# Kernel optimization log

Hardware: AMD Instinct MI355X
Metric: run time of the kernel (lower is better)

The kernel has to match this reference:

```python
import jax, jax.numpy as jnp
import numpy as np

HIDDEN = 2048
FFN = 1024
NUM_EXPERTS = 64
TOP_K = 8
TOTAL_EXPERTS = NUM_EXPERTS + TOP_K  # trash-can experts appended


def setup_inputs() -> dict:
    key = jax.random.key(0)
    ks = jax.random.split(key, 5)
    hidden_states = jax.random.normal(ks[0], (4, 2048, HIDDEN), dtype=jnp.float32)
    # gate: [total_experts, hidden]
    gate_w = jax.random.normal(ks[1], (TOTAL_EXPERTS, HIDDEN), dtype=jnp.float32) * 0.02
    # OlmoeMLP (SwiGLU): gate_proj, up_proj: [E, hidden, ffn]; down_proj: [E, ffn, hidden]
    w_gate = jax.random.normal(ks[2], (NUM_EXPERTS, HIDDEN, FFN), dtype=jnp.float32) * 0.02
    w_up = jax.random.normal(ks[3], (NUM_EXPERTS, HIDDEN, FFN), dtype=jnp.float32) * 0.02
    w_down = jax.random.normal(ks[4], (NUM_EXPERTS, FFN, HIDDEN), dtype=jnp.float32) * 0.02
    return {"hidden_states": hidden_states, "gate_w": gate_w,
            "w_gate": w_gate, "w_up": w_up, "w_down": w_down}


def _moe_forward(hidden_states, gate_w, w_gate, w_up, w_down):
    b, s, h = hidden_states.shape
    x = hidden_states.reshape(-1, h)  # [T, H]
    router_logits = x @ gate_w.T  # [T, total_experts]
    routing_weights = jax.nn.softmax(router_logits.astype(jnp.float32), axis=-1)
    topk_w, topk_idx = jax.lax.top_k(routing_weights, TOP_K)  # [T, K]
    # norm_topk_prob = False -> no renorm
    topk_w = topk_w.astype(hidden_states.dtype)

    # Dense-equivalent combine honoring sparsity via per-expert mask-weighted sum:
    # combine_w[t, e] = sum of topk weights where topk_idx==e, zero for trash experts.
    onehot = jax.nn.one_hot(topk_idx, TOTAL_EXPERTS, dtype=topk_w.dtype)  # [T,K,E_tot]
    combine_w = jnp.einsum('tk,tke->te', topk_w, onehot)[:, :NUM_EXPERTS]  # [T,E]

    # Grouped expert compute (vectorized over experts).
    # For correctness baseline we compute each expert on all tokens and weight;
    # zero weights kill non-routed tokens (same math as gather/scatter).
    def one_expert(wg, wu, wd, w_col):
        inter = jax.nn.silu(x @ wg) * (x @ wu)  # [T, FFN]
        return (inter @ wd) * w_col[:, None]    # [T, H]

    out = jnp.zeros_like(x)
    # scan over experts to cap peak memory at one [T,FFN] intermediate
    def body(acc, args):
        wg, wu, wd, w_col = args
        return acc + one_expert(wg, wu, wd, w_col), None
    out, _ = jax.lax.scan(body, out, (w_gate, w_up, w_down, combine_w.T))
    return out.reshape(b, s, h), router_logits


def reference(hidden_states, gate_w, w_gate, w_up, w_down):
    return _moe_forward(hidden_states, gate_w, w_gate, w_up, w_down)
```

## Files before the change

### kernel.cpp

```cpp
#include <hip/hip_runtime.h>
#include <hip/hip_bf16.h>
#include <stdint.h>

#define T_TOK 8192
#define HID   2048
#define FFN   1024
#define NEXP  64
#define ETOT  72
#define NPAD  80
#define TOPK  8
#define NASSIGN (T_TOK*TOPK)

typedef unsigned short u16;
typedef __bf16 bf16;
typedef bf16 bf16x8 __attribute__((ext_vector_type(8)));
typedef float f32x4 __attribute__((ext_vector_type(4)));

typedef const __attribute__((address_space(1))) void* gp_t;
typedef __attribute__((address_space(3))) void* lp_t;

__device__ __forceinline__ void gload16(const void* g, void* lds) {
  __builtin_amdgcn_global_load_lds((gp_t)g, (lp_t)lds, 16, 0, 0);
}
__device__ __forceinline__ f32x4 mfma16(bf16x8 a, bf16x8 b, f32x4 c) {
  return __builtin_amdgcn_mfma_f32_16x16x32_bf16(a, b, c, 0, 0, 0);
}

union U8 { bf16 h[8]; uint4 u; };
union U2 { bf16 h[2]; unsigned int u; };

__global__ void k_prep_x(const float* __restrict__ x, u16* __restrict__ xh,
                         u16* __restrict__ xl, int n8) {
  int i = blockIdx.x * blockDim.x + threadIdx.x;
  int stride = gridDim.x * blockDim.x;
  for (; i < n8; i += stride) {
    const float4* p = (const float4*)(x + (size_t)i * 8);
    float4 a = p[0], b = p[1];
    float f[8] = {a.x,a.y,a.z,a.w,b.x,b.y,b.z,b.w};
    U8 hh, ll;
#pragma unroll
    for (int j = 0; j < 8; j++) {
      bf16 h = (bf16)f[j];
      hh.h[j] = h;
      ll.h[j] = (bf16)(f[j] - (float)h);
    }
    ((uint4*)xh)[i] = hh.u;
    ((uint4*)xl)[i] = ll.u;
  }
}

__global__ void k_prep_gate(const float* __restrict__ gw, u16* __restrict__ gh,
                            u16* __restrict__ gl) {
  int e = blockIdx.x;
  for (int k8 = threadIdx.x; k8 < HID/8; k8 += blockDim.x) {
    U8 hh, ll;
    if (e < ETOT) {
      const float4* p = (const float4*)(gw + (size_t)e*HID + k8*8);
      float4 a = p[0], b = p[1];
      float f[8] = {a.x,a.y,a.z,a.w,b.x,b.y,b.z,b.w};
#pragma unroll
      for (int j = 0; j < 8; j++) {
        bf16 h = (bf16)f[j]; hh.h[j] = h; ll.h[j] = (bf16)(f[j]-(float)h);
      }
    } else {
      hh.u = make_uint4(0,0,0,0); ll.u = make_uint4(0,0,0,0);
    }
    ((uint4*)gh)[(size_t)e*(HID/8) + k8] = hh.u;
    ((uint4*)gl)[(size_t)e*(HID/8) + k8] = ll.u;
  }
}

__global__ void k_convT(const float* __restrict__ src, u16* __restrict__ dst,
                        int R, int C) {
  int e = blockIdx.z;
  src += (size_t)e * R * C;
  dst += (size_t)e * R * C;
  int c0 = blockIdx.x * 64, r0 = blockIdx.y * 128;
  __shared__ u16 t[64 * 132];
  int tid = threadIdx.x;
  int rr = tid >> 4, cc = (tid & 15) * 4;
#pragma unroll
  for (int it = 0; it < 8; it++) {
    int r = it * 16 + rr;
    float4 v = *(const float4*)(src + (size_t)(r0 + r) * C + c0 + cc);
    const float* f = &v.x;
#pragma unroll
    for (int i = 0; i < 4; i++) {
      U2 u; u.h[0] = (bf16)f[i]; u.h[1] = (bf16)0.f;
      t[(cc + i) * 132 + r] = (u16)(u.u & 0xffffu);
    }
  }
  __syncthreads();
  int n = tid >> 2, kb = (tid & 3) * 32;
  u16* drow = dst + (size_t)(c0 + n) * R + r0 + kb;
  const u16* srow = &t[n * 132 + kb];
#pragma unroll
  for (int j = 0; j < 2; j++) {
    uint2 a = *(const uint2*)&srow[j*16 + 0];
    uint2 b = *(const uint2*)&srow[j*16 + 4];
    uint2 c = *(const uint2*)&srow[j*16 + 8];
    uint2 d = *(const uint2*)&srow[j*16 + 12];
    *(uint4*)&drow[j*16]     = make_uint4(a.x, a.y, b.x, b.y);
    *(uint4*)&drow[j*16 + 8] = make_uint4(c.x, c.y, d.x, d.y);
  }
}

__global__ void k_router(const u16* __restrict__ xh, const u16* __restrict__ xl,
                         const u16* __restrict__ gh, const u16* __restrict__ gl,
                         float* __restrict__ logits_out, int* __restrict__ tk_idx,
                         float* __restrict__ tk_w, int* __restrict__ counts) {
  __shared__ u16 la_h[64*32], la_l[64*32], lb_h[NPAD*32], lb_l[NPAD*32];
  __shared__ float llog[64*NPAD];
  int tid = threadIdx.x, lane = tid & 63, wid = tid >> 6;
  int t0 = blockIdx.x * 64;
  int rsub = lane >> 2, csub = lane & 3;
  f32x4 acc[5] = {};
#pragma unroll 1
  for (int k0 = 0; k0 < HID; k0 += 32) {
    int arow = wid*16 + rsub;
    gload16(xh + (size_t)(t0+arow)*HID + k0 + csub*8, &la_h[wid*512]);
    gload16(xl + (size_t)(t0+arow)*HID + k0 + csub*8, &la_l[wid*512]);
    int brow = wid*16 + rsub;
    gload16(gh + (size_t)brow*HID + k0 + csub*8, &lb_h[wid*512]);
    gload16(gl + (size_t)brow*HID + k0 + csub*8, &lb_l[wid*512]);
    if (wid == 0) gload16(gh + (size_t)(64+rsub)*HID + k0 + csub*8, &lb_h[4*512]);
    if (wid == 1) gload16(gl + (size_t)(64+rsub)*HID + k0 + csub*8, &lb_l[4*512]);
    __syncthreads();
    int ar = wid*16 + (lane & 15);
    int ks = lane >> 4;
    bf16x8 ah = *(const bf16x8*)&la_h[ar*32 + ks*8];
    bf16x8 al = *(const bf16x8*)&la_l[ar*32 + ks*8];
#pragma unroll
    for (int nf = 0; nf < 5; nf++) {
      int br = nf*16 + (lane & 15);
      bf16x8 bh = *(const bf16x8*)&lb_h[br*32 + ks*8];
      bf16x8 bl = *(const bf16x8*)&lb_l[br*32 + ks*8];
      acc[nf] = mfma16(ah, bh, acc[nf]);
      acc[nf] = mfma16(ah, bl, acc[nf]);
      acc[nf] = mfma16(al, bh, acc[nf]);
    }
    __syncthreads();
  }
  {
    int q = lane >> 4, c = lane & 15;
#pragma unroll
    for (int nf = 0; nf < 5; nf++)
#pragma unroll
      for (int r = 0; r < 4; r++)
        llog[(wid*16 + q*4 + r)*NPAD + nf*16 + c] = acc[nf][r];
  }
  __syncthreads();
  if (tid < 64) {
    int t = t0 + tid;
    float* lg = &llog[tid*NPAD];
    float m = -1e30f;
    for (int e = 0; e < ETOT; e++) {
      float v = lg[e];
      logits_out[(size_t)t*ETOT + e] = v;
      m = fmaxf(m, v);
    }
    float s = 0.f;
    for (int e = 0; e < ETOT; e++) s += __expf(lg[e] - m);
    uint64_t m0 = 0; unsigned int m1 = 0;
    for (int k = 0; k < TOPK; k++) {
      float best = -1e30f; int bi = 0;
      for (int e = 0; e < ETOT; e++) {
        bool used = (e < 64) ? ((m0 >> e) & 1) : ((m1 >> (e-64)) & 1);
        float v = lg[e];
        if (!used && v > best) { best = v; bi = e; }
      }
      if (bi < 64) m0 |= (1ull << bi); else m1 |= (1u << (bi-64));
      tk_idx[t*TOPK + k] = bi;
      tk_w[t*TOPK + k] = __expf(best - m) / s;
      if (bi < NEXP) atomicAdd(&counts[bi], 1);
    }
  }
}

__global__ void k_scan(const int* __restrict__ counts, int* __restrict__ offsets,
                       int* __restrict__ cursors) {
  if (threadIdx.x == 0) {
    int s = 0;
    for (int e = 0; e < NEXP; e++) { offsets[e] = s; cursors[e] = s; s += counts[e]; }
  }
}

__global__ void k_build(const int* __restrict__ tk_idx, const float* __restrict__ tk_w,
                        int* __restrict__ cursors, int* __restrict__ rows,
                        float* __restrict__ rwgt, int* __restrict__ slots) {
  int t = blockIdx.x * blockDim.x + threadIdx.x;
  if (t >= T_TOK) return;
#pragma unroll
  for (int k = 0; k < TOPK; k++) {
    int e = tk_idx[t*TOPK + k];
    if (e < NEXP) {
      int p = atomicAdd(&cursors[e], 1);
      rows[p] = t;
      rwgt[p] = tk_w[t*TOPK + k];
      slots[t*TOPK + k] = p;
    } else {
      slots[t*TOPK + k] = -1;
    }
  }
}

#define FRAG_COMPUTE(LAP, LBP) do { \
    bf16x8 afr[4], bfr[4]; \
    _Pragma("unroll") \
    for (int i = 0; i < 4; i++) { \
      int row = wm + i*16 + (lane & 15); \
      int ch = (lane >> 4) ^ ((row >> 1) & 3); \
      afr[i] = *(const bf16x8*)&(LAP)[row*32 + ch*8]; \
      int n = wn + i*16 + (lane & 15); \
      int chb = (lane >> 4) ^ ((n >> 1) & 3); \
      bfr[i] = *(const bf16x8*)&(LBP)[n*32 + chb*8]; \
    } \
    _Pragma("unroll") \
    for (int nf = 0; nf < 4; nf++) \
      _Pragma("unroll") \
      for (int mf = 0; mf < 4; mf++) \
        acc[mf][nf] = mfma16(afr[mf], bfr[nf], acc[mf][nf]); \
  } while (0)

#define BK64_LOOP(KDIM) \
    _Pragma("unroll 1") \
    for (int k0 = 0; k0 < (KDIM); k0 += 64) { \
      gload16(ga1 + k0, &la[wid*512]); \
      gload16(ga2 + k0, &la[(wid+4)*512]); \
      gload16(gb1 + k0, &lb[wid*512]); \
      gload16(gb2 + k0, &lb[(wid+4)*512]); \
      gload16(ga1 + k0 + 32, &la[4096 + wid*512]); \
      gload16(ga2 + k0 + 32, &la[4096 + (wid+4)*512]); \
      gload16(gb1 + k0 + 32, &lb[4096 + wid*512]); \
      gload16(gb2 + k0 + 32, &lb[4096 + (wid+4)*512]); \
      __syncthreads(); \
      FRAG_COMPUTE(la, lb); \
      FRAG_COMPUTE((la + 4096), (lb + 4096)); \
      __syncthreads(); \
    }

__launch_bounds__(256, 4)
__global__ void k_gate(const u16* __restrict__ xh, const u16* __restrict__ wT,
                       const int* __restrict__ counts, const int* __restrict__ offsets,
                       const int* __restrict__ rows, u16* __restrict__ gout) {
  int wgid = blockIdx.x;
  int xcd = wgid & 7, slot = wgid >> 3;
  int m = slot & 7, q = slot >> 3;
  int g = xcd * 64 + q;
  int e = g >> 3, nb = g & 7;
  int cnt = counts[e];
  if (cnt == 0) return;
  int off = offsets[e];
  int n0 = nb * 128;
  int tid = threadIdx.x, lane = tid & 63, wid = tid >> 6;
  int wm = (wid >> 1) * 64, wn = (wid & 1) * 64;
  __shared__ __align__(16) char smem[32768];
  u16* la = (u16*)smem;
  u16* lb = (u16*)(smem + 16384);
  u16* lout = (u16*)smem;
  int rsub = lane >> 2, csub = lane & 3;
  int swzc = csub ^ ((rsub >> 1) & 3);
  int nr1 = wid*16 + rsub, nr2 = nr1 + 64;
  const u16* gb1 = wT + ((size_t)e*FFN + n0 + nr1)*HID + swzc*8;
  const u16* gb2 = wT + ((size_t)e*FFN + n0 + nr2)*HID + swzc*8;

  for (int m0 = m * 128; m0 < cnt; m0 += 1024) {
    int tok1 = (m0 + nr1 < cnt) ? rows[off + m0 + nr1] : 0;
    int tok2 = (m0 + nr2 < cnt) ? rows[off + m0 + nr2] : 0;
    const u16* ga1 = xh + (size_t)tok1*HID + swzc*8;
    const u16* ga2 = xh + (size_t)tok2*HID + swzc*8;
    f32x4 acc[4][4] = {};
    BK64_LOOP(HID)
#pragma unroll
    for (int pass = 0; pass < 2; pass++) {
      if ((wid >> 1) == pass) {
#pragma unroll
        for (int mf = 0; mf < 4; mf++)
#pragma unroll
          for (int nf = 0; nf < 4; nf++)
#pragma unroll
            for (int r = 0; r < 4; r++) {
              int row = mf*16 + (lane >> 4)*4 + r;
              int col = wn + nf*16 + (lane & 15);
              U2 t; t.h[0] = (bf16)acc[mf][nf][r]; t.h[1] = (bf16)0.f;
              lout[row*128 + col] = (u16)(t.u & 0xffffu);
            }
      }
      __syncthreads();
      for (int idx = tid; idx < 1024; idx += 256) {
        int row = idx >> 4, c16 = idx & 15;
        int grow = m0 + pass*64 + row;
        if (grow < cnt) {
          uint4 v = *(const uint4*)&lout[row*128 + c16*8];
          *(uint4*)&gout[(size_t)(off + grow)*FFN + n0 + c16*8] = v;
        }
      }
      __syncthreads();
    }
  }
}

__launch_bounds__(256, 4)
__global__ void k_up(const u16* __restrict__ xh, const u16* __restrict__ wT,
                     const int* __restrict__ counts, const int* __restrict__ offsets,
                     const int* __restrict__ rows, u16* __restrict__ inter) {
  int wgid = blockIdx.x;
  int xcd = wgid & 7, slot = wgid >> 3;
  int m = slot & 7, q = slot >> 3;
  int g = xcd * 64 + q;
  int e = g >> 3, nb = g & 7;
  int cnt = counts[e];
  if (cnt == 0) return;
  int off = offsets[e];
  int n0 = nb * 128;
  int tid = threadIdx.x, lane = tid & 63, wid = tid >> 6;
  int wm = (wid >> 1) * 64, wn = (wid & 1) * 64;
  __shared__ __align__(16) char smem[32768];
  u16* la = (u16*)smem;
  u16* lb = (u16*)(smem + 16384);
  u16* lg = (u16*)smem;
  u16* lout = (u16*)(smem + 16384);
  int rsub = lane >> 2, csub = lane & 3;
  int swzc = csub ^ ((rsub >> 1) & 3);
  int nr1 = wid*16 + rsub, nr2 = nr1 + 64;
  const u16* gb1 = wT + ((size_t)e*FFN + n0 + nr1)*HID + swzc*8;
  const u16* gb2 = wT + ((size_t)e*FFN + n0 + nr2)*HID + swzc*8;

  for (int m0 = m * 128; m0 < cnt; m0 += 1024) {
    int tok1 = (m0 + nr1 < cnt) ? rows[off + m0 + nr1] : 0;
    int tok2 = (m0 + nr2 < cnt) ? rows[off + m0 + nr2] : 0;
    const u16* ga1 = xh + (size_t)tok1*HID + swzc*8;
    const u16* ga2 = xh + (size_t)tok2*HID + swzc*8;
    f32x4 acc[4][4] = {};
    BK64_LOOP(HID)
#pragma unroll
    for (int pass = 0; pass < 2; pass++) {
      for (int idx = tid; idx < 1024; idx += 256) {
        int row = idx >> 4, c16 = idx & 15;
        int grow = m0 + pass*64 + row;
        uint4 v = make_uint4(0,0,0,0);
        if (grow < cnt)
          v = *(const uint4*)&inter[(size_t)(off + grow)*FFN + n0 + c16*8];
        *(uint4*)&lg[row*128 + c16*8] = v;
      }
      __syncthreads();
      if ((wid >> 1) == pass) {
#pragma unroll
        for (int mf = 0; mf < 4; mf++)
#pragma unroll
          for (int nf = 0; nf < 4; nf++)
#pragma unroll
            for (int r = 0; r < 4; r++) {
              int row = mf*16 + (lane >> 4)*4 + r;
              int col = wn + nf*16 + (lane & 15);
              U2 gv; gv.u = (unsigned int)lg[row*128 + col];
              float gg = (float)gv.h[0];
              float v = gg / (1.f + __expf(-gg)) * acc[mf][nf][r];
              U2 t; t.h[0] = (bf16)v; t.h[1] = (bf16)0.f;
              lout[row*128 + col] = (u16)(t.u & 0xffffu);
            }
      }
      __syncthreads();
      for (int idx = tid; idx < 1024; idx += 256) {
        int row = idx >> 4, c16 = idx & 15;
        int grow = m0 + pass*64 + row;
        if (grow < cnt) {
          uint4 v = *(const uint4*)&lout[row*128 + c16*8];
          *(uint4*)&inter[(size_t)(off + grow)*FFN + n0 + c16*8] = v;
        }
      }
      __syncthreads();
    }
  }
}

__launch_bounds__(256, 4)
__global__ void k_expert_down(const u16* __restrict__ inter, const u16* __restrict__ wdT,
                              const int* __restrict__ counts, const int* __restrict__ offsets,
                              const float* __restrict__ rwgt, u16* __restrict__ dscratch) {
  int wgid = blockIdx.x;
  int xcd = wgid & 7, slot = wgid >> 3;
  int m = slot & 3, q = slot >> 2;
  int g = xcd * 128 + q;
  int e = g >> 4, nb = g & 15;
  int cnt = counts[e];
  if (cnt == 0) return;
  int off = offsets[e];
  int n0 = nb * 128;
  int tid = threadIdx.x, lane = tid & 63, wid = tid >> 6;
  int wm = (wid >> 1) * 64, wn = (wid & 1) * 64;
  __shared__ __align__(16) char smem[32768];
  u16* la = (u16*)smem;
  u16* lb = (u16*)(smem + 16384);
  u16* lout = (u16*)smem;
  __shared__ float rw_l[128];
  int rsub = lane >> 2, csub = lane & 3;
  int swzc = csub ^ ((rsub >> 1) & 3);
  int nr1 = wid*16 + rsub, nr2 = nr1 + 64;
  const u16* gb1 = wdT + ((size_t)e*HID + n0 + nr1)*FFN + swzc*8;
  const u16* gb2 = wdT + ((size_t)e*HID + n0 + nr2)*FFN + swzc*8;

  for (int m0 = m * 128; m0 < cnt; m0 += 512) {
    __syncthreads();
    if (tid < 128) {
      int r = m0 + tid;
      rw_l[tid] = (r < cnt) ? rwgt[off + r] : 0.f;
    }
    const u16* ga1 = inter + (size_t)(off + m0 + nr1)*FFN + swzc*8;
    const u16* ga2 = inter + (size_t)(off + m0 + nr2)*FFN + swzc*8;
    f32x4 acc[4][4] = {};
    BK64_LOOP(FFN)
#pragma unroll
    for (int pass = 0; pass < 2; pass++) {
      if ((wid >> 1) == pass) {
#pragma unroll
        for (int mf = 0; mf < 4; mf++)
#pragma unroll
          for (int nf = 0; nf < 4; nf++)
#pragma unroll
            for (int r = 0; r < 4; r++) {
              int row = mf*16 + (lane >> 4)*4 + r;
              int col = wn + nf*16 + (lane & 15);
              float w = rw_l[pass*64 + row];
              U2 t; t.h[0] = (bf16)(w * acc[mf][nf][r]); t.h[1] = (bf16)0.f;
              lout[row*128 + col] = (u16)(t.u & 0xffffu);
            }
      }
      __syncthreads();
      for (int idx = tid; idx < 1024; idx += 256) {
        int row = idx >> 4, c16 = idx & 15;
        int grow = m0 + pass*64 + row;
        if (grow < cnt) {
          uint4 v = *(const uint4*)&lout[row*128 + c16*8];
          *(uint4*)&dscratch[(size_t)(off + grow)*HID + n0 + c16*8] = v;
        }
      }
      __syncthreads();
    }
  }
}

__global__ void k_combine(const u16* __restrict__ dscratch, const int* __restrict__ slots,
                          float* __restrict__ out) {
  int t = blockIdx.x;
  int tid = threadIdx.x;
  __shared__ int sl[TOPK];
  if (tid < TOPK) sl[tid] = slots[t*TOPK + tid];
  __syncthreads();
  int c = tid * 8;
  float acc[8] = {0.f,0.f,0.f,0.f,0.f,0.f,0.f,0.f};
#pragma unroll
  for (int k = 0; k < TOPK; k++) {
    int p = sl[k];
    if (p >= 0) {
      bf16x8 v = *(const bf16x8*)&dscratch[(size_t)p*HID + c];
#pragma unroll
      for (int i = 0; i < 8; i++) acc[i] += (float)v[i];
    }
  }
  float4 o0 = make_float4(acc[0], acc[1], acc[2], acc[3]);
  float4 o1 = make_float4(acc[4], acc[5], acc[6], acc[7]);
  *(float4*)&out[(size_t)t*HID + c]     = o0;
  *(float4*)&out[(size_t)t*HID + c + 4] = o1;
}

extern "C" void kernel_launch(void* const* d_in, const int* in_sizes, int n_in,
                              void* d_out, int out_size, void* d_ws, size_t ws_size,
                              hipStream_t stream) {
  const float* x      = (const float*)d_in[0];
  const float* gate_w = (const float*)d_in[1];
  const float* wg     = (const float*)d_in[2];
  const float* wu     = (const float*)d_in[3];
  const float* wd     = (const float*)d_in[4];
  float* out = (float*)d_out;
  float* logits_out = out + (size_t)T_TOK * HID;

  char* w = (char*)d_ws;
  u16* xh = (u16*)w;            w += (size_t)T_TOK*HID*2;
  u16* xl = (u16*)w;            w += (size_t)T_TOK*HID*2;
  u16* gh = (u16*)w;            w += (size_t)NPAD*HID*2;
  u16* gl = (u16*)w;            w += (size_t)NPAD*HID*2;
  int* tk_idx = (int*)w;        w += (size_t)T_TOK*TOPK*4;
  float* tk_w = (float*)w;      w += (size_t)T_TOK*TOPK*4;
  int* counts = (int*)w;        w += 256;
  int* offsets = (int*)w;       w += 256;
  int* cursors = (int*)w;       w += 256;
  int* rows = (int*)w;          w += (size_t)NASSIGN*4;
  float* rwgt = (float*)w;      w += (size_t)NASSIGN*4;
  int* slots = (int*)w;         w += (size_t)NASSIGN*4;
  u16* inter = (u16*)w;         w += ((size_t)NASSIGN + 256)*FFN*2;
  u16* dscratch = (u16*)w;      w += (size_t)NASSIGN*HID*2;
  u16* wgT = (u16*)w;           w += (size_t)NEXP*FFN*HID*2;
  u16* wuT = (u16*)w;           w += (size_t)NEXP*FFN*HID*2;
  u16* wdT = (u16*)w;

  hipMemsetAsync(counts, 0, 256, stream);

  k_prep_x<<<2048, 256, 0, stream>>>(x, xh, xl, T_TOK*HID/8);
  k_prep_gate<<<NPAD, 256, 0, stream>>>(gate_w, gh, gl);
  k_router<<<T_TOK/64, 256, 0, stream>>>(xh, xl, gh, gl, logits_out, tk_idx, tk_w, counts);
  k_scan<<<1, 64, 0, stream>>>(counts, offsets, cursors);
  k_build<<<T_TOK/256, 256, 0, stream>>>(tk_idx, tk_w, cursors, rows, rwgt, slots);

  k_convT<<<dim3(FFN/64, HID/128, NEXP), 256, 0, stream>>>(wg, wgT, HID, FFN);
  k_convT<<<dim3(FFN/64, HID/128, NEXP), 256, 0, stream>>>(wu, wuT, HID, FFN);
  k_convT<<<dim3(HID/64, FFN/128, NEXP), 256, 0, stream>>>(wd, wdT, FFN, HID);

  k_gate<<<4096, 256, 0, stream>>>(xh, wgT, counts, offsets, rows, inter);
  k_up<<<4096, 256, 0, stream>>>(xh, wuT, counts, offsets, rows, inter);
  k_expert_down<<<4096, 256, 0, stream>>>(inter, wdT, counts, offsets, rwgt, dscratch);
  k_combine<<<T_TOK, 256, 0, stream>>>(dscratch, slots, out);
}
```

Measured before the change: 1.762 ms.

## Fuse weight transpose-conversion into router and expert GEMM kernels for overlap

Removes the three standalone weight conversion kernels. Their tiles are folded into the preceding compute kernels as extra workgroups: router plus gate-weight conversion, gate GEMM plus up-weight conversion, up GEMM plus down-weight conversion. This lets memory-bound conversion overlap with compute-bound work and drops launch gaps. It also switches the conversion to nontemporal loads and stores. The cost is interleaved block scheduling, which can contend for bandwidth and occupancy with the GEMM blocks, and the router's launch bounds drop to 2.

```diff
diff --git a/kernel.cpp b/kernel.cpp
--- a/kernel.cpp
+++ b/kernel.cpp
@@ -15,6 +15,7 @@
 typedef __bf16 bf16;
 typedef bf16 bf16x8 __attribute__((ext_vector_type(8)));
 typedef float f32x4 __attribute__((ext_vector_type(4)));
+typedef unsigned int u32x4 __attribute__((ext_vector_type(4)));
 
 typedef const __attribute__((address_space(1))) void* gp_t;
 typedef __attribute__((address_space(3))) void* lp_t;
@@ -28,6 +29,52 @@
 
 union U8 { bf16 h[8]; uint4 u; };
 union U2 { bf16 h[2]; unsigned int u; };
+union UV { u32x4 v; float f[4]; };
+
+__device__ __forceinline__ void conv_tile4(const float* __restrict__ src0,
+                                           u16* __restrict__ dst0,
+                                           int R, int C, int conv_id, u16* t) {
+  int tid = threadIdx.x;
+  int tiles_c = C >> 6;
+  int rr = tid >> 4, cc = (tid & 15) * 4;
+#pragma unroll 1
+  for (int j = 0; j < 4; j++) {
+    int tile = conv_id * 4 + j;
+    int e = tile >> 8, rem = tile & 255;
+    int bx = rem % tiles_c, by = rem / tiles_c;
+    const float* src = src0 + (size_t)e * R * C;
+    u16* dst = dst0 + (size_t)e * R * C;
+    int c0 = bx * 64, r0 = by * 128;
+    __syncthreads();
+#pragma unroll
+    for (int it = 0; it < 8; it++) {
+      int r = it * 16 + rr;
+      UV uv;
+      uv.v = __builtin_nontemporal_load(
+          (const u32x4*)(src + (size_t)(r0 + r) * C + c0 + cc));
+#pragma unroll
+      for (int i = 0; i < 4; i++) {
+        U2 u; u.h[0] = (bf16)uv.f[i]; u.h[1] = (bf16)0.f;
+        t[(cc + i) * 132 + r] = (u16)(u.u & 0xffffu);
+      }
+    }
+    __syncthreads();
+    int n = tid >> 2, kb = (tid & 3) * 32;
+    u16* drow = dst + (size_t)(c0 + n) * R + r0 + kb;
+    const u16* srow = &t[n * 132 + kb];
+#pragma unroll
+    for (int jj = 0; jj < 2; jj++) {
+      uint2 a = *(const uint2*)&srow[jj*16 + 0];
+      uint2 b = *(const uint2*)&srow[jj*16 + 4];
+      uint2 c = *(const uint2*)&srow[jj*16 + 8];
+      uint2 d = *(const uint2*)&srow[jj*16 + 12];
+      u32x4 o0 = {a.x, a.y, b.x, b.y};
+      u32x4 o1 = {c.x, c.y, d.x, d.y};
+      __builtin_nontemporal_store(o0, (u32x4*)&drow[jj*16]);
+      __builtin_nontemporal_store(o1, (u32x4*)&drow[jj*16 + 8]);
+    }
+  }
+}
 
 __global__ void k_prep_x(const float* __restrict__ x, u16* __restrict__ xh,
                          u16* __restrict__ xl, int n8) {
@@ -70,49 +117,25 @@
   }
 }
 
-__global__ void k_convT(const float* __restrict__ src, u16* __restrict__ dst,
-                        int R, int C) {
-  int e = blockIdx.z;
-  src += (size_t)e * R * C;
-  dst += (size_t)e * R * C;
-  int c0 = blockIdx.x * 64, r0 = blockIdx.y * 128;
-  __shared__ u16 t[64 * 132];
-  int tid = threadIdx.x;
-  int rr = tid >> 4, cc = (tid & 15) * 4;
-#pragma unroll
-  for (int it = 0; it < 8; it++) {
-    int r = it * 16 + rr;
-    float4 v = *(const float4*)(src + (size_t)(r0 + r) * C + c0 + cc);
-    const float* f = &v.x;
-#pragma unroll
-    for (int i = 0; i < 4; i++) {
-      U2 u; u.h[0] = (bf16)f[i]; u.h[1] = (bf16)0.f;
-      t[(cc + i) * 132 + r] = (u16)(u.u & 0xffffu);
-    }
-  }
-  __syncthreads();
-  int n = tid >> 2, kb = (tid & 3) * 32;
-  u16* drow = dst + (size_t)(c0 + n) * R + r0 + kb;
-  const u16* srow = &t[n * 132 + kb];
-#pragma unroll
-  for (int j = 0; j < 2; j++) {
-    uint2 a = *(const uint2*)&srow[j*16 + 0];
-    uint2 b = *(const uint2*)&srow[j*16 + 4];
-    uint2 c = *(const uint2*)&srow[j*16 + 8];
-    uint2 d = *(const uint2*)&srow[j*16 + 12];
-    *(uint4*)&drow[j*16]     = make_uint4(a.x, a.y, b.x, b.y);
-    *(uint4*)&drow[j*16 + 8] = make_uint4(c.x, c.y, d.x, d.y);
-  }
-}
-
-__global__ void k_router(const u16* __restrict__ xh, const u16* __restrict__ xl,
-                         const u16* __restrict__ gh, const u16* __restrict__ gl,
-                         float* __restrict__ logits_out, int* __restrict__ tk_idx,
-                         float* __restrict__ tk_w, int* __restrict__ counts) {
-  __shared__ u16 la_h[64*32], la_l[64*32], lb_h[NPAD*32], lb_l[NPAD*32];
-  __shared__ float llog[64*NPAD];
+__launch_bounds__(256, 2)
+__global__ void k_router_convwg(const u16* __restrict__ xh, const u16* __restrict__ xl,
+                                const u16* __restrict__ gh, const u16* __restrict__ gl,
+                                float* __restrict__ logits_out, int* __restrict__ tk_idx,
+                                float* __restrict__ tk_w, int* __restrict__ counts,
+                                const float* __restrict__ wg_src, u16* __restrict__ wgT) {
+  __shared__ __align__(16) char smem[38912];
+  int bid = blockIdx.x;
+  if (bid >= 128) {
+    conv_tile4(wg_src, wgT, HID, FFN, bid - 128, (u16*)smem);
+    return;
+  }
+  u16* la_h = (u16*)smem;
+  u16* la_l = (u16*)(smem + 4096);
+  u16* lb_h = (u16*)(smem + 8192);
+  u16* lb_l = (u16*)(smem + 13312);
+  float* llog = (float*)(smem + 18432);
   int tid = threadIdx.x, lane = tid & 63, wid = tid >> 6;
-  int t0 = blockIdx.x * 64;
+  int t0 = bid * 64;
   int rsub = lane >> 2, csub = lane & 3;
   f32x4 acc[5] = {};
 #pragma unroll 1
@@ -240,10 +263,18 @@
     }
 
 __launch_bounds__(256, 4)
-__global__ void k_gate(const u16* __restrict__ xh, const u16* __restrict__ wT,
-                       const int* __restrict__ counts, const int* __restrict__ offsets,
-                       const int* __restrict__ rows, u16* __restrict__ gout) {
-  int wgid = blockIdx.x;
+__global__ void k_gate_convwu(const u16* __restrict__ xh, const u16* __restrict__ wT,
+                              const int* __restrict__ counts, const int* __restrict__ offsets,
+                              const int* __restrict__ rows, u16* __restrict__ gout,
+                              const float* __restrict__ wu_src, u16* __restrict__ wuT) {
+  __shared__ __align__(16) char smem[32768];
+  int bid = blockIdx.x;
+  int octet = bid >> 3, lane8 = bid & 7;
+  if (octet & 1) {
+    conv_tile4(wu_src, wuT, HID, FFN, ((octet >> 1) << 3) | lane8, (u16*)smem);
+    return;
+  }
+  int wgid = ((octet >> 1) << 3) | lane8;
   int xcd = wgid & 7, slot = wgid >> 3;
   int m = slot & 7, q = slot >> 3;
   int g = xcd * 64 + q;
@@ -254,7 +285,6 @@
   int n0 = nb * 128;
   int tid = threadIdx.x, lane = tid & 63, wid = tid >> 6;
   int wm = (wid >> 1) * 64, wn = (wid & 1) * 64;
-  __shared__ __align__(16) char smem[32768];
   u16* la = (u16*)smem;
   u16* lb = (u16*)(smem + 16384);
   u16* lout = (u16*)smem;
@@ -301,10 +331,18 @@
 }
 
 __launch_bounds__(256, 4)
-__global__ void k_up(const u16* __restrict__ xh, const u16* __restrict__ wT,
-                     const int* __restrict__ counts, const int* __restrict__ offsets,
-                     const int* __restrict__ rows, u16* __restrict__ inter) {
-  int wgid = blockIdx.x;
+__global__ void k_up_convwd(const u16* __restrict__ xh, const u16* __restrict__ wT,
+                            const int* __restrict__ counts, const int* __restrict__ offsets,
+                            const int* __restrict__ rows, u16* __restrict__ inter,
+                            const float* __restrict__ wd_src, u16* __restrict__ wdT) {
+  __shared__ __align__(16) char smem[32768];
+  int bid = blockIdx.x;
+  int octet = bid >> 3, lane8 = bid & 7;
+  if (octet & 1) {
+    conv_tile4(wd_src, wdT, FFN, HID, ((octet >> 1) << 3) | lane8, (u16*)smem);
+    return;
+  }
+  int wgid = ((octet >> 1) << 3) | lane8;
   int xcd = wgid & 7, slot = wgid >> 3;
   int m = slot & 7, q = slot >> 3;
   int g = xcd * 64 + q;
@@ -315,7 +353,6 @@
   int n0 = nb * 128;
   int tid = threadIdx.x, lane = tid & 63, wid = tid >> 6;
   int wm = (wid >> 1) * 64, wn = (wid & 1) * 64;
-  __shared__ __align__(16) char smem[32768];
   u16* la = (u16*)smem;
   u16* lb = (u16*)(smem + 16384);
   u16* lg = (u16*)smem;
@@ -498,16 +535,13 @@
 
   k_prep_x<<<2048, 256, 0, stream>>>(x, xh, xl, T_TOK*HID/8);
   k_prep_gate<<<NPAD, 256, 0, stream>>>(gate_w, gh, gl);
-  k_router<<<T_TOK/64, 256, 0, stream>>>(xh, xl, gh, gl, logits_out, tk_idx, tk_w, counts);
+  k_router_convwg<<<128 + 4096, 256, 0, stream>>>(
+      xh, xl, gh, gl, logits_out, tk_idx, tk_w, counts, wg, wgT);
   k_scan<<<1, 64, 0, stream>>>(counts, offsets, cursors);
   k_build<<<T_TOK/256, 256, 0, stream>>>(tk_idx, tk_w, cursors, rows, rwgt, slots);
 
-  k_convT<<<dim3(FFN/64, HID/128, NEXP), 256, 0, stream>>>(wg, wgT, HID, FFN);
-  k_convT<<<dim3(FFN/64, HID/128, NEXP), 256, 0, stream>>>(wu, wuT, HID, FFN);
-  k_convT<<<dim3(HID/64, FFN/128, NEXP), 256, 0, stream>>>(wd, wdT, FFN, HID);
-
-  k_gate<<<4096, 256, 0, stream>>>(xh, wgT, counts, offsets, rows, inter);
-  k_up<<<4096, 256, 0, stream>>>(xh, wuT, counts, offsets, rows, inter);
+  k_gate_convwu<<<8192, 256, 0, stream>>>(xh, wgT, counts, offsets, rows, inter, wu, wuT);
+  k_up_convwd<<<8192, 256, 0, stream>>>(xh, wuT, counts, offsets, rows, inter, wd, wdT);
   k_expert_down<<<4096, 256, 0, stream>>>(inter, wdT, counts, offsets, rwgt, dscratch);
   k_combine<<<T_TOK, 256, 0, stream>>>(dscratch, slots, out);
 }
```

Result: slower. 2.499 ms (+41.8%).

## Double-buffer K-loop with async LDS prefetch and vmcnt waits

Applied to the files above, without the earlier changes.

Replaces the synchronous BK=64 loop, which loads both halves and then computes, with a BK=32 double-buffered pipeline in all three grouped GEMM kernels. The next K-slice is issued into the alternate LDS buffer before computing the current one, and explicit s_waitcnt vmcnt(4) waits only for the older loads. This aims to overlap global-to-LDS transfer with MFMA work, at the cost of twice as many barriers per unit of K and reliance on manual vmcnt accounting for correctness.

```diff
diff --git a/kernel.cpp b/kernel.cpp
--- a/kernel.cpp
+++ b/kernel.cpp
@@ -222,22 +222,30 @@
         acc[mf][nf] = mfma16(afr[mf], bfr[nf], acc[mf][nf]); \
   } while (0)
 
-#define BK64_LOOP(KDIM) \
+#define STAGE32(B, K0) do { \
+    gload16(ga1 + (K0), &la[(B)*4096 + wid*512]); \
+    gload16(ga2 + (K0), &la[(B)*4096 + (wid+4)*512]); \
+    gload16(gb1 + (K0), &lb[(B)*4096 + wid*512]); \
+    gload16(gb2 + (K0), &lb[(B)*4096 + (wid+4)*512]); \
+  } while (0)
+
+#define BK32_PIPE(KDIM) do { \
+    int b = 0; \
+    STAGE32(0, 0); \
     _Pragma("unroll 1") \
-    for (int k0 = 0; k0 < (KDIM); k0 += 64) { \
-      gload16(ga1 + k0, &la[wid*512]); \
-      gload16(ga2 + k0, &la[(wid+4)*512]); \
-      gload16(gb1 + k0, &lb[wid*512]); \
-      gload16(gb2 + k0, &lb[(wid+4)*512]); \
-      gload16(ga1 + k0 + 32, &la[4096 + wid*512]); \
-      gload16(ga2 + k0 + 32, &la[4096 + (wid+4)*512]); \
-      gload16(gb1 + k0 + 32, &lb[4096 + wid*512]); \
-      gload16(gb2 + k0 + 32, &lb[4096 + (wid+4)*512]); \
-      __syncthreads(); \
-      FRAG_COMPUTE(la, lb); \
-      FRAG_COMPUTE((la + 4096), (lb + 4096)); \
-      __syncthreads(); \
-    }
+    for (int k0 = 0; k0 < (KDIM); k0 += 32) { \
+      if (k0 + 32 < (KDIM)) { \
+        STAGE32(b ^ 1, k0 + 32); \
+        asm volatile("s_waitcnt vmcnt(4)" ::: "memory"); \
+      } else { \
+        asm volatile("s_waitcnt vmcnt(0)" ::: "memory"); \
+      } \
+      __builtin_amdgcn_s_barrier(); \
+      FRAG_COMPUTE((la + b*4096), (lb + b*4096)); \
+      __builtin_amdgcn_s_barrier(); \
+      b ^= 1; \
+    } \
+  } while (0)
 
 __launch_bounds__(256, 4)
 __global__ void k_gate(const u16* __restrict__ xh, const u16* __restrict__ wT,
@@ -270,7 +278,8 @@
     const u16* ga1 = xh + (size_t)tok1*HID + swzc*8;
     const u16* ga2 = xh + (size_t)tok2*HID + swzc*8;
     f32x4 acc[4][4] = {};
-    BK64_LOOP(HID)
+    BK32_PIPE(HID);
+    __syncthreads();
 #pragma unroll
     for (int pass = 0; pass < 2; pass++) {
       if ((wid >> 1) == pass) {
@@ -332,7 +341,8 @@
     const u16* ga1 = xh + (size_t)tok1*HID + swzc*8;
     const u16* ga2 = xh + (size_t)tok2*HID + swzc*8;
     f32x4 acc[4][4] = {};
-    BK64_LOOP(HID)
+    BK32_PIPE(HID);
+    __syncthreads();
 #pragma unroll
     for (int pass = 0; pass < 2; pass++) {
       for (int idx = tid; idx < 1024; idx += 256) {
@@ -409,7 +419,8 @@
     const u16* ga1 = inter + (size_t)(off + m0 + nr1)*FFN + swzc*8;
     const u16* ga2 = inter + (size_t)(off + m0 + nr2)*FFN + swzc*8;
     f32x4 acc[4][4] = {};
-    BK64_LOOP(FFN)
+    BK32_PIPE(FFN);
+    __syncthreads();
 #pragma unroll
     for (int pass = 0; pass < 2; pass++) {
       if ((wid >> 1) == pass) {
```

Result: slower. 1.855 ms (+5.3%).

## Fuse gate and up expert GEMMs into one kernel keeping gate in registers

Applied to the files above, without the earlier changes.

Merges the separate gate and up projection kernels into a single kernel that runs the gate GEMM, packs its result to bf16 in registers, then runs the up GEMM and applies SiLU-multiply before storing the intermediate. This removes the round-trip of the gate output through global memory, one kernel launch, and the repeated row-index setup. The extra live registers lower the launch-bounds occupancy target from 4 to 3. Separately, the transpose kernel's LDS row padding changes from 132 to 134 to alter the bank-conflict pattern.

```diff
diff --git a/kernel.cpp b/kernel.cpp
--- a/kernel.cpp
+++ b/kernel.cpp
@@ -76,7 +76,7 @@
   src += (size_t)e * R * C;
   dst += (size_t)e * R * C;
   int c0 = blockIdx.x * 64, r0 = blockIdx.y * 128;
-  __shared__ u16 t[64 * 132];
+  __shared__ u16 t[64 * 134];
   int tid = threadIdx.x;
   int rr = tid >> 4, cc = (tid & 15) * 4;
 #pragma unroll
@@ -87,13 +87,13 @@
 #pragma unroll
     for (int i = 0; i < 4; i++) {
       U2 u; u.h[0] = (bf16)f[i]; u.h[1] = (bf16)0.f;
-      t[(cc + i) * 132 + r] = (u16)(u.u & 0xffffu);
+      t[(cc + i) * 134 + r] = (u16)(u.u & 0xffffu);
     }
   }
   __syncthreads();
   int n = tid >> 2, kb = (tid & 3) * 32;
   u16* drow = dst + (size_t)(c0 + n) * R + r0 + kb;
-  const u16* srow = &t[n * 132 + kb];
+  const u16* srow = &t[n * 134 + kb];
 #pragma unroll
   for (int j = 0; j < 2; j++) {
     uint2 a = *(const uint2*)&srow[j*16 + 0];
@@ -239,10 +239,11 @@
       __syncthreads(); \
     }
 
-__launch_bounds__(256, 4)
-__global__ void k_gate(const u16* __restrict__ xh, const u16* __restrict__ wT,
-                       const int* __restrict__ counts, const int* __restrict__ offsets,
-                       const int* __restrict__ rows, u16* __restrict__ gout) {
+__launch_bounds__(256, 3)
+__global__ void k_gateup(const u16* __restrict__ xh, const u16* __restrict__ wgT,
+                         const u16* __restrict__ wuT, const int* __restrict__ counts,
+                         const int* __restrict__ offsets, const int* __restrict__ rows,
+                         u16* __restrict__ inter) {
   int wgid = blockIdx.x;
   int xcd = wgid & 7, slot = wgid >> 3;
   int m = slot & 7, q = slot >> 3;
@@ -261,8 +262,10 @@
   int rsub = lane >> 2, csub = lane & 3;
   int swzc = csub ^ ((rsub >> 1) & 3);
   int nr1 = wid*16 + rsub, nr2 = nr1 + 64;
-  const u16* gb1 = wT + ((size_t)e*FFN + n0 + nr1)*HID + swzc*8;
-  const u16* gb2 = wT + ((size_t)e*FFN + n0 + nr2)*HID + swzc*8;
+  const u16* gbg1 = wgT + ((size_t)e*FFN + n0 + nr1)*HID + swzc*8;
+  const u16* gbg2 = wgT + ((size_t)e*FFN + n0 + nr2)*HID + swzc*8;
+  const u16* gbu1 = wuT + ((size_t)e*FFN + n0 + nr1)*HID + swzc*8;
+  const u16* gbu2 = wuT + ((size_t)e*FFN + n0 + nr2)*HID + swzc*8;
 
   for (int m0 = m * 128; m0 < cnt; m0 += 1024) {
     int tok1 = (m0 + nr1 < cnt) ? rows[off + m0 + nr1] : 0;
@@ -270,7 +273,29 @@
     const u16* ga1 = xh + (size_t)tok1*HID + swzc*8;
     const u16* ga2 = xh + (size_t)tok2*HID + swzc*8;
     f32x4 acc[4][4] = {};
-    BK64_LOOP(HID)
+
+    {
+      const u16* gb1 = gbg1;
+      const u16* gb2 = gbg2;
+      BK64_LOOP(HID)
+    }
+    unsigned int gpk[4][4][2];
+#pragma unroll
+    for (int mf = 0; mf < 4; mf++)
+#pragma unroll
+      for (int nf = 0; nf < 4; nf++) {
+        U2 a, b;
+        a.h[0] = (bf16)acc[mf][nf][0]; a.h[1] = (bf16)acc[mf][nf][1];
+        b.h[0] = (bf16)acc[mf][nf][2]; b.h[1] = (bf16)acc[mf][nf][3];
+        gpk[mf][nf][0] = a.u; gpk[mf][nf][1] = b.u;
+        acc[mf][nf] = (f32x4){0.f, 0.f, 0.f, 0.f};
+      }
+    {
+      const u16* gb1 = gbu1;
+      const u16* gb2 = gbu2;
+      BK64_LOOP(HID)
+    }
+
 #pragma unroll
     for (int pass = 0; pass < 2; pass++) {
       if ((wid >> 1) == pass) {
@@ -280,82 +305,11 @@
           for (int nf = 0; nf < 4; nf++)
 #pragma unroll
             for (int r = 0; r < 4; r++) {
+              U2 gv; gv.u = gpk[mf][nf][r >> 1];
+              float gg = (float)gv.h[r & 1];
+              float v = gg / (1.f + __expf(-gg)) * acc[mf][nf][r];
               int row = mf*16 + (lane >> 4)*4 + r;
               int col = wn + nf*16 + (lane & 15);
-              U2 t; t.h[0] = (bf16)acc[mf][nf][r]; t.h[1] = (bf16)0.f;
-              lout[row*128 + col] = (u16)(t.u & 0xffffu);
-            }
-      }
-      __syncthreads();
-      for (int idx = tid; idx < 1024; idx += 256) {
-        int row = idx >> 4, c16 = idx & 15;
-        int grow = m0 + pass*64 + row;
-        if (grow < cnt) {
-          uint4 v = *(const uint4*)&lout[row*128 + c16*8];
-          *(uint4*)&gout[(size_t)(off + grow)*FFN + n0 + c16*8] = v;
-        }
-      }
-      __syncthreads();
-    }
-  }
-}
-
-__launch_bounds__(256, 4)
-__global__ void k_up(const u16* __restrict__ xh, const u16* __restrict__ wT,
-                     const int* __restrict__ counts, const int* __restrict__ offsets,
-                     const int* __restrict__ rows, u16* __restrict__ inter) {
-  int wgid = blockIdx.x;
-  int xcd = wgid & 7, slot = wgid >> 3;
-  int m = slot & 7, q = slot >> 3;
-  int g = xcd * 64 + q;
-  int e = g >> 3, nb = g & 7;
-  int cnt = counts[e];
-  if (cnt == 0) return;
-  int off = offsets[e];
-  int n0 = nb * 128;
-  int tid = threadIdx.x, lane = tid & 63, wid = tid >> 6;
-  int wm = (wid >> 1) * 64, wn = (wid & 1) * 64;
-  __shared__ __align__(16) char smem[32768];
-  u16* la = (u16*)smem;
-  u16* lb = (u16*)(smem + 16384);
-  u16* lg = (u16*)smem;
-  u16* lout = (u16*)(smem + 16384);
-  int rsub = lane >> 2, csub = lane & 3;
-  int swzc = csub ^ ((rsub >> 1) & 3);
-  int nr1 = wid*16 + rsub, nr2 = nr1 + 64;
-  const u16* gb1 = wT + ((size_t)e*FFN + n0 + nr1)*HID + swzc*8;
-  const u16* gb2 = wT + ((size_t)e*FFN + n0 + nr2)*HID + swzc*8;
-
-  for (int m0 = m * 128; m0 < cnt; m0 += 1024) {
-    int tok1 = (m0 + nr1 < cnt) ? rows[off + m0 + nr1] : 0;
-    int tok2 = (m0 + nr2 < cnt) ? rows[off + m0 + nr2] : 0;
-    const u16* ga1 = xh + (size_t)tok1*HID + swzc*8;
-    const u16* ga2 = xh + (size_t)tok2*HID + swzc*8;
-    f32x4 acc[4][4] = {};
-    BK64_LOOP(HID)
-#pragma unroll
-    for (int pass = 0; pass < 2; pass++) {
-      for (int idx = tid; idx < 1024; idx += 256) {
-        int row = idx >> 4, c16 = idx & 15;
-        int grow = m0 + pass*64 + row;
-        uint4 v = make_uint4(0,0,0,0);
-        if (grow < cnt)
-          v = *(const uint4*)&inter[(size_t)(off + grow)*FFN + n0 + c16*8];
-        *(uint4*)&lg[row*128 + c16*8] = v;
-      }
-      __syncthreads();
-      if ((wid >> 1) == pass) {
-#pragma unroll
-        for (int mf = 0; mf < 4; mf++)
-#pragma unroll
-          for (int nf = 0; nf < 4; nf++)
-#pragma unroll
-            for (int r = 0; r < 4; r++) {
-              int row = mf*16 + (lane >> 4)*4 + r;
-              int col = wn + nf*16 + (lane & 15);
-              U2 gv; gv.u = (unsigned int)lg[row*128 + col];
-              float gg = (float)gv.h[0];
-              float v = gg / (1.f + __expf(-gg)) * acc[mf][nf][r];
               U2 t; t.h[0] = (bf16)v; t.h[1] = (bf16)0.f;
               lout[row*128 + col] = (u16)(t.u & 0xffffu);
             }
@@ -506,8 +460,7 @@
   k_convT<<<dim3(FFN/64, HID/128, NEXP), 256, 0, stream>>>(wu, wuT, HID, FFN);
   k_convT<<<dim3(HID/64, FFN/128, NEXP), 256, 0, stream>>>(wd, wdT, FFN, HID);
 
-  k_gate<<<4096, 256, 0, stream>>>(xh, wgT, counts, offsets, rows, inter);
-  k_up<<<4096, 256, 0, stream>>>(xh, wuT, counts, offsets, rows, inter);
+  k_gateup<<<4096, 256, 0, stream>>>(xh, wgT, wuT, counts, offsets, rows, inter);
   k_expert_down<<<4096, 256, 0, stream>>>(inter, wdT, counts, offsets, rwgt, dscratch);
   k_combine<<<T_TOK, 256, 0, stream>>>(dscratch, slots, out);
 }
```

After: 1.805 ms. +2.4%, slower.
